# Kernel tuning notes

Hardware: AMD Instinct MI355X
Metric: run time of the kernel (lower is better)

The kernel has to match this reference:

```python
import jax, jax.numpy as jnp
import numpy as np

EPS = 1e-3  # tfa GroupNormalization default epsilon
H = 8       # num heads


def group_norm(x, gamma, beta):
    # x: [..., E]; per-sample group norm over each group of head_dim channels
    lead, E = x.shape[:-1], x.shape[-1]
    D = E // H
    xg = x.reshape(lead + (H, D))
    mu = xg.mean(-1, keepdims=True)
    var = xg.var(-1, keepdims=True)
    xg = (xg - mu) * jax.lax.rsqrt(var + EPS)
    xg = xg * gamma.reshape(H, D) + beta.reshape(H, D)
    return xg.reshape(lead + (E,))


def in_proj(x, W, b, gamma, beta):
    # Dense -> CELU(alpha=1) == ELU -> GroupNorm(groups=H)
    return group_norm(jax.nn.elu(x @ W + b), gamma, beta)


def setup_inputs() -> dict:
    B, M, E, MID = 16, 2048, 1024, 64
    D = E // H
    ks = jax.random.split(jax.random.key(0), 16)
    w = lambda k, shape: jax.random.normal(k, shape, jnp.float32) * 0.02
    inp = {
        "query": jax.random.normal(ks[0], (B, E), jnp.float32),
        "key": jax.random.normal(ks[1], (B * M, E), jnp.float32),
        "mask": jnp.ones((B, M), jnp.float32),
        "value1": jax.random.normal(ks[2], (B, E), jnp.float32),
        "value2": jax.random.normal(ks[3], (B * M, E), jnp.float32),
        # four in-projection layers: Dense(E,E) + GroupNorm gamma/beta
        "Wq": w(ks[4], (E, E)), "bq": jnp.zeros((E,), jnp.float32), "gq": jnp.ones((E,), jnp.float32), "Bq": jnp.zeros((E,), jnp.float32),
        "Wk": w(ks[5], (E, E)), "bk": jnp.zeros((E,), jnp.float32), "gk": jnp.ones((E,), jnp.float32), "Bk": jnp.zeros((E,), jnp.float32),
        "Wv1": w(ks[6], (E, E)), "bv1": jnp.zeros((E,), jnp.float32), "gv1": jnp.ones((E,), jnp.float32), "Bv1": jnp.zeros((E,), jnp.float32),
        "Wv2": w(ks[7], (E, E)), "bv2": jnp.zeros((E,), jnp.float32), "gv2": jnp.ones((E,), jnp.float32), "Bv2": jnp.zeros((E,), jnp.float32),
        # XLASCAtt: basic Dense(head_dim->64)+ReLU; last Dense(64->1); last2 Dense(64->head_dim)
        "Wb": w(ks[8], (D, MID)), "bb": jnp.zeros((MID,), jnp.float32),
        "Wl1": w(ks[9], (MID, 1)), "bl1": jnp.zeros((1,), jnp.float32),
        "Wl2": w(ks[10], (MID, D)), "bl2": jnp.zeros((D,), jnp.float32),
    }
    return inp


def reference(query, key, mask, value1, value2,
              Wq, bq, gq, Bq, Wk, bk, gk, Bk,
              Wv1, bv1, gv1, Bv1, Wv2, bv2, gv2, Bv2,
              Wb, bb, Wl1, bl1, Wl2, bl2):
    B, E = query.shape
    D = E // H
    # in-projections
    q = in_proj(query, Wq, bq, gq, Bq).reshape(B, H, D)            # [B,H,D]
    v1 = in_proj(value1, Wv1, bv1, gv1, Bv1).reshape(B, H, D)      # [B,H,D]
    k = in_proj(key, Wk, bk, gk, Bk).reshape(B, -1, H, D).transpose(0, 2, 1, 3)       # [B,H,M,D]
    v2 = in_proj(value2, Wv2, bv2, gv2, Bv2).reshape(B, -1, H, D).transpose(0, 2, 1, 3)  # [B,H,M,D]

    # low-rank bilinear attention map: elementwise q*k per head
    att_map = q[:, :, None, :] * k                                 # [B,H,M,D]
    basic = jax.nn.relu(att_map @ Wb + bb)                         # [B,H,M,MID]

    # masked mean-pool over memory positions
    m_ext = mask[:, None, :, None]                                 # [B,1,M,1]
    pool = (basic * m_ext).sum(-2) / m_ext.sum(-2)                 # [B,H,MID]

    # spatial attention (softmax over M) and channel gate (sigmoid)
    alpha_sp = (basic @ Wl1 + bl1)[..., 0]                         # [B,H,M]
    alpha_sp = jnp.where(mask[:, None, :] == 0, -1e9, alpha_sp)
    alpha_sp = jax.nn.softmax(alpha_sp, axis=-1)
    alpha_ch = jax.nn.sigmoid(pool @ Wl2 + bl2)                    # [B,H,D]

    v2_agg = jnp.einsum('bhm,bhmd->bhd', alpha_sp, v2)             # [B,H,D]
    attn = v1 * v2_agg * alpha_ch                                  # [B,H,D]
    return attn.reshape(B, H * D)
```

## Files before the change

kernel.cpp:

```cpp
#include <hip/hip_runtime.h>
#include <hip/hip_bf16.h>
#include <math.h>

typedef __attribute__((ext_vector_type(8))) short bf16x8;
typedef __attribute__((ext_vector_type(4))) float f32x4;
typedef __attribute__((ext_vector_type(8))) unsigned short u16x8;

typedef const float* fptr;
typedef const unsigned short* bfp;

__device__ inline float b2f(unsigned short u) {
    union { unsigned int i; float f; } v; v.i = ((unsigned int)u) << 16; return v.f;
}
__device__ inline unsigned short f2b(float x) {
    __hip_bfloat16 h = __float2bfloat16(x);
    return *(unsigned short*)&h;
}
__device__ inline float elu_f(float x) { return x > 0.f ? x : __expf(x) - 1.f; }

__device__ inline void load_lds16(const void* g, void* l) {
    __builtin_amdgcn_global_load_lds(
        (const __attribute__((address_space(1))) unsigned int*)g,
        (__attribute__((address_space(3))) unsigned int*)l, 16, 0, 0);
}

__global__ __launch_bounds__(256) void prep(
    fptr key, fptr value2, unsigned short* AbfK, unsigned short* AbfV2,
    fptr Wk, fptr Wv2, unsigned short* WtK, unsigned short* WtV2,
    fptr Wb, unsigned short* Wbt,
    fptr query, fptr Wq, fptr bq, fptr gq, fptr Bq,
    fptr value1, fptr Wv1, fptr bv1, fptr gv1, fptr Bv1,
    float* qws, float* v1ws)
{
    __shared__ __align__(16) char smem[16640];
    int blk = blockIdx.x, t = threadIdx.x;

    if (blk == 0) {
        unsigned short* tb = (unsigned short*)smem;
        for (int i = 0; i < 32; i++) {
            int idx = i * 256 + t;
            tb[(idx & 63) * 128 + (idx >> 6)] = f2b(Wb[idx]);
        }
        __syncthreads();
        for (int i = 0; i < 4; i++) {
            int o = (i * 256 + t) * 8;
            *(u16x8*)&Wbt[o] = *(const u16x8*)&tb[o];
        }
        return;
    }
    if (blk < 257) {
        float* xs = (float*)smem;
        float (*part)[128] = (float (*)[128])(smem + 4096);
        float (*r4)[2] = (float (*)[2])(smem + 4096 + 1024);
        int idx = blk - 1;
        int hgrp = idx & 7;
        int row  = (idx >> 3) & 15;
        int which = idx >> 7;
        fptr x  = which ? value1 : query;
        fptr W  = which ? Wv1 : Wq;
        fptr bi = which ? bv1 : bq;
        fptr g  = which ? gv1 : gq;
        fptr be = which ? Bv1 : Bq;
        float* outp = which ? v1ws : qws;
        int lane = t & 63, wv = t >> 6;
        for (int i = t; i < 1024; i += 256) xs[i] = x[row * 1024 + i];
        __syncthreads();
        int cl = t & 127, kh = t >> 7;
        int col = hgrp * 128 + cl;
        float acc = 0.f;
        const float* wp = W + (size_t)(kh * 512) * 1024 + col;
        for (int k = 0; k < 512; k++) acc += xs[kh * 512 + k] * wp[(size_t)k * 1024];
        part[kh][cl] = acc;
        __syncthreads();
        float e = 0.f;
        if (t < 128) e = elu_f(part[0][t] + part[1][t] + bi[col]);
        float s = e, ss = e * e;
        for (int m = 32; m > 0; m >>= 1) { s += __shfl_xor(s, m); ss += __shfl_xor(ss, m); }
        if (lane == 0) { r4[wv][0] = s; r4[wv][1] = ss; }
        __syncthreads();
        float S  = r4[0][0] + r4[1][0] + r4[2][0] + r4[3][0];
        float SS = r4[0][1] + r4[1][1] + r4[2][1] + r4[3][1];
        float mean = S * (1.f / 128.f);
        float var  = SS * (1.f / 128.f) - mean * mean;
        float inv  = rsqrtf(var + 1e-3f);
        if (t < 128) outp[row * 1024 + col] = (e - mean) * inv * g[col] + be[col];
        return;
    }
    if (blk < 769) {
        float (*tl)[65] = (float (*)[65])smem;
        int idx = blk - 257;
        fptr W = (idx >> 8) ? Wv2 : Wk;
        unsigned short* Wt = (idx >> 8) ? WtV2 : WtK;
        int k0 = ((idx >> 4) & 15) * 64, n0 = (idx & 15) * 64;
        #pragma unroll
        for (int i = 0; i < 16; i++) {
            int kl = i * 4 + (t >> 6), nl = t & 63;
            tl[kl][nl] = W[(size_t)(k0 + kl) * 1024 + n0 + nl];
        }
        __syncthreads();
        #pragma unroll
        for (int i = 0; i < 16; i++) {
            int nl = i * 4 + (t >> 6), kl = t & 63;
            Wt[(size_t)(n0 + nl) * 1024 + k0 + kl] = f2b(tl[kl][nl]);
        }
        return;
    }
    {
        int idx = blk - 769;
        fptr A = (idx < 16384) ? key : value2;
        unsigned short* B = (idx < 16384) ? AbfK : AbfV2;
        size_t e = ((size_t)(idx & 16383) * 256 + t) * 8;
        const float4* ap = (const float4*)(A + e);
        float4 a0 = ap[0], a1 = ap[1];
        u16x8 p = { f2b(a0.x), f2b(a0.y), f2b(a0.z), f2b(a0.w),
                    f2b(a1.x), f2b(a1.y), f2b(a1.z), f2b(a1.w) };
        *(u16x8*)(B + e) = p;
    }
}

__global__ __launch_bounds__(256, 3) void gemm_fused(
    bfp AK, bfp WtK, fptr bkp, fptr gkp, fptr Bkp,
    bfp AV, bfp WtV, fptr bvp, fptr gvp, fptr Bvp,
    bfp Wbt, const float* qws, fptr maskp, fptr bbp, fptr Wl1, fptr bl1,
    float* logits, float* poolpart, __hip_bfloat16* Z)
{
    __shared__ __align__(16) unsigned short pool[17408];
    unsigned short (*As)[128][32] = (unsigned short (*)[128][32])pool;
    unsigned short (*Bs)[128][32] = (unsigned short (*)[128][32])(pool + 8192);
    unsigned short (*Tt)[136]     = (unsigned short (*)[136])pool;
    __shared__ float sstat[128][2][2];
    __shared__ float masksh[128];
    __shared__ float poolred[4][64];

    int bid = blockIdx.x;
    int xcd = bid & 7;
    int seq = bid >> 3;
    int grp = seq >> 3;
    int h   = seq & 7;
    int which = grp >> 5;
    int rowtile = xcd * 32 + (grp & 31);

    int r0 = rowtile * 128;
    int n0 = h * 128;
    int b  = r0 >> 11;
    int mloc = r0 & 2047;
    int mt = rowtile & 15;
    int t = threadIdx.x, lane = t & 63, w = t >> 6;
    int c = lane & 15, q = lane >> 4;
    int rowbase = (w & 1) * 64, colbase = (w >> 1) * 64;

    bfp A    = which ? AV  : AK;
    bfp Wt   = which ? WtV : WtK;
    fptr bias = which ? bvp : bkp;
    fptr g    = which ? gvp : gkp;
    fptr be   = which ? Bvp : Bkp;

    if (which == 0 && t < 128) masksh[t] = maskp[r0 + t];

    f32x4 acc[4][4];
    const f32x4 fzero = {0.f, 0.f, 0.f, 0.f};
    #pragma unroll
    for (int i = 0; i < 4; i++)
        #pragma unroll
        for (int j = 0; j < 4; j++) acc[i][j] = fzero;

    int srow = lane >> 2;
    int sseg = (lane & 3) * 8;
    const unsigned short* ag = A  + (size_t)(r0 + w * 32 + srow) * 1024 + sseg;
    const unsigned short* bg = Wt + (size_t)(n0 + w * 32 + srow) * 1024 + sseg;

    for (int k0 = 0; k0 < 1024; k0 += 64) {
        load_lds16(ag + k0,                  &As[0][w * 32][0]);
        load_lds16(ag + k0 + 16 * 1024,      &As[0][w * 32 + 16][0]);
        load_lds16(ag + k0 + 32,             &As[1][w * 32][0]);
        load_lds16(ag + k0 + 32 + 16 * 1024, &As[1][w * 32 + 16][0]);
        load_lds16(bg + k0,                  &Bs[0][w * 32][0]);
        load_lds16(bg + k0 + 16 * 1024,      &Bs[0][w * 32 + 16][0]);
        load_lds16(bg + k0 + 32,             &Bs[1][w * 32][0]);
        load_lds16(bg + k0 + 32 + 16 * 1024, &Bs[1][w * 32 + 16][0]);
        __syncthreads();
        #pragma unroll
        for (int p = 0; p < 2; p++) {
            bf16x8 af[4], bfv[4];
            #pragma unroll
            for (int i = 0; i < 4; i++) af[i]  = *(const bf16x8*)&As[p][rowbase + i * 16 + c][q * 8];
            #pragma unroll
            for (int j = 0; j < 4; j++) bfv[j] = *(const bf16x8*)&Bs[p][colbase + j * 16 + c][q * 8];
            #pragma unroll
            for (int i = 0; i < 4; i++)
                #pragma unroll
                for (int j = 0; j < 4; j++)
                    acc[i][j] = __builtin_amdgcn_mfma_f32_16x16x32_bf16(af[i], bfv[j], acc[i][j], 0, 0, 0);
        }
        __syncthreads();
    }

    float bcol[4], gcol[4], Bcol[4];
    #pragma unroll
    for (int j = 0; j < 4; j++) {
        int cg = n0 + colbase + j * 16 + c;
        bcol[j] = bias[cg]; gcol[j] = g[cg]; Bcol[j] = be[cg];
    }
    #pragma unroll
    for (int i = 0; i < 4; i++)
        #pragma unroll
        for (int j = 0; j < 4; j++)
            #pragma unroll
            for (int r = 0; r < 4; r++)
                acc[i][j][r] = elu_f(acc[i][j][r] + bcol[j]);
    #pragma unroll
    for (int i = 0; i < 4; i++) {
        #pragma unroll
        for (int r = 0; r < 4; r++) {
            float s  = acc[i][0][r] + acc[i][1][r] + acc[i][2][r] + acc[i][3][r];
            float ss = acc[i][0][r] * acc[i][0][r] + acc[i][1][r] * acc[i][1][r]
                     + acc[i][2][r] * acc[i][2][r] + acc[i][3][r] * acc[i][3][r];
            for (int m = 1; m < 16; m <<= 1) { s += __shfl_xor(s, m); ss += __shfl_xor(ss, m); }
            if (c == 0) {
                int rl = rowbase + i * 16 + q * 4 + r;
                sstat[rl][w >> 1][0] = s;
                sstat[rl][w >> 1][1] = ss;
            }
        }
    }
    __syncthreads();
    #pragma unroll
    for (int i = 0; i < 4; i++) {
        #pragma unroll
        for (int r = 0; r < 4; r++) {
            int rl = rowbase + i * 16 + q * 4 + r;
            float S  = sstat[rl][0][0] + sstat[rl][1][0];
            float SS = sstat[rl][0][1] + sstat[rl][1][1];
            float mean = S * (1.f / 128.f);
            float var  = SS * (1.f / 128.f) - mean * mean;
            float inv  = rsqrtf(var + 1e-3f);
            #pragma unroll
            for (int j = 0; j < 4; j++) {
                int cl = colbase + j * 16 + c;
                float v = (acc[i][j][r] - mean) * inv * gcol[j] + Bcol[j];
                if (which == 0) Tt[rl][cl] = f2b(v);
                else Z[(size_t)(r0 + rl) * 1024 + n0 + cl] = __float2bfloat16(v);
            }
        }
    }
    if (which != 0) return;
    __syncthreads();

    const float* qrow = qws + b * 1024 + h * 128;
    f32x4 acc2[2][4];
    #pragma unroll
    for (int i = 0; i < 2; i++)
        #pragma unroll
        for (int j = 0; j < 4; j++) acc2[i][j] = fzero;
    #pragma unroll
    for (int s = 0; s < 4; s++) {
        bf16x8 af2[2], bfv[4];
        float qv[8];
        #pragma unroll
        for (int e = 0; e < 8; e++) qv[e] = qrow[s * 32 + q * 8 + e];
        #pragma unroll
        for (int i = 0; i < 2; i++)
            af2[i] = *(const bf16x8*)&Tt[w * 32 + i * 16 + c][s * 32 + q * 8];
        #pragma unroll
        for (int j = 0; j < 4; j++) {
            bf16x8 wv = *(const bf16x8*)&Wbt[(j * 16 + c) * 128 + s * 32 + q * 8];
            bf16x8 bv;
            #pragma unroll
            for (int e = 0; e < 8; e++)
                bv[e] = (short)f2b(b2f((unsigned short)wv[e]) * qv[e]);
            bfv[j] = bv;
        }
        #pragma unroll
        for (int i = 0; i < 2; i++)
            #pragma unroll
            for (int j = 0; j < 4; j++)
                acc2[i][j] = __builtin_amdgcn_mfma_f32_16x16x32_bf16(af2[i], bfv[j], acc2[i][j], 0, 0, 0);
    }

    float bbs[4], wl1s[4];
    #pragma unroll
    for (int j = 0; j < 4; j++) { bbs[j] = bbp[j * 16 + c]; wl1s[j] = Wl1[j * 16 + c]; }
    float bl1v = bl1[0];
    float pp[4] = {0.f, 0.f, 0.f, 0.f};
    #pragma unroll
    for (int i = 0; i < 2; i++) {
        #pragma unroll
        for (int r = 0; r < 4; r++) {
            int ml = w * 32 + i * 16 + q * 4 + r;
            float mv = masksh[ml];
            float lg = 0.f;
            #pragma unroll
            for (int j = 0; j < 4; j++) {
                float basic = fmaxf(acc2[i][j][r] + bbs[j], 0.f);
                lg += basic * wl1s[j];
                pp[j] += basic * mv;
            }
            lg += __shfl_xor(lg, 1); lg += __shfl_xor(lg, 2);
            lg += __shfl_xor(lg, 4); lg += __shfl_xor(lg, 8);
            if (c == 0)
                logits[((size_t)(b * 8 + h)) * 2048 + mloc + ml] = lg + bl1v;
        }
    }
    #pragma unroll
    for (int j = 0; j < 4; j++) {
        pp[j] += __shfl_xor(pp[j], 16);
        pp[j] += __shfl_xor(pp[j], 32);
    }
    if (lane < 16) {
        #pragma unroll
        for (int j = 0; j < 4; j++) poolred[w][j * 16 + c] = pp[j];
    }
    __syncthreads();
    if (t < 64) {
        float p = poolred[0][t] + poolred[1][t] + poolred[2][t] + poolred[3][t];
        poolpart[((size_t)((b * 8 + h) * 16 + mt)) * 64 + t] = p;
    }
}

__global__ __launch_bounds__(512) void finalize_fused(
    const float* logits, const float* poolpart, fptr maskp,
    const __hip_bfloat16* v2buf, const float* v1ws,
    fptr Wl2, fptr bl2, float* out)
{
    __shared__ float alph[2048];
    __shared__ float red[8];
    __shared__ float redm[8];
    __shared__ float pools[64];
    __shared__ float ach[128];
    __shared__ float redl[8][128];
    int h = blockIdx.x, b = blockIdx.y;
    int t = threadIdx.x, lane = t & 63, wv = t >> 6;

    const float* lg = logits + (size_t)(b * 8 + h) * 2048;
    float msum_l = 0.f, mx_l = -1e30f;
    for (int i = t; i < 2048; i += 512) {
        float mv = maskp[b * 2048 + i];
        msum_l += mv;
        float v = (mv == 0.f) ? -1e9f : lg[i];
        alph[i] = v;
        mx_l = fmaxf(mx_l, v);
    }
    for (int mm = 32; mm > 0; mm >>= 1) {
        msum_l += __shfl_xor(msum_l, mm);
        mx_l = fmaxf(mx_l, __shfl_xor(mx_l, mm));
    }
    if (lane == 0) { red[wv] = msum_l; redm[wv] = mx_l; }
    __syncthreads();
    float msum = 0.f, mx = -1e30f;
    #pragma unroll
    for (int i = 0; i < 8; i++) { msum += red[i]; mx = fmaxf(mx, redm[i]); }

    float se = 0.f;
    for (int i = t; i < 2048; i += 512) {
        float e = __expf(alph[i] - mx);
        alph[i] = e;
        se += e;
    }
    for (int mm = 32; mm > 0; mm >>= 1) se += __shfl_xor(se, mm);
    __syncthreads();
    if (lane == 0) red[wv] = se;
    __syncthreads();
    float S = 0.f;
    #pragma unroll
    for (int i = 0; i < 8; i++) S += red[i];
    float invS = 1.f / S;
    for (int i = t; i < 2048; i += 512) alph[i] *= invS;

    if (t < 64) {
        const float* pq = poolpart + ((size_t)(b * 8 + h) * 16) * 64 + t;
        float p = 0.f;
        for (int pt = 0; pt < 16; pt++) p += pq[pt * 64];
        pools[t] = p / msum;
    }
    __syncthreads();
    if (t < 128) {
        float s2 = bl2[t];
        for (int mid = 0; mid < 64; mid++) s2 += pools[mid] * Wl2[mid * 128 + t];
        ach[t] = 1.f / (1.f + __expf(-s2));
    }
    __syncthreads();

    int mo = lane >> 4, d8 = (lane & 15) * 8;
    float acc[8] = {};
    for (int it = 0; it < 64; it++) {
        int m = it * 32 + wv * 4 + mo;
        bf16x8 v8 = *(const bf16x8*)&v2buf[((size_t)(b * 2048 + m)) * 1024 + h * 128 + d8];
        float a = alph[m];
        #pragma unroll
        for (int j = 0; j < 8; j++)
            acc[j] += a * b2f(((unsigned short*)&v8)[j]);
    }
    #pragma unroll
    for (int j = 0; j < 8; j++) {
        acc[j] += __shfl_xor(acc[j], 16);
        acc[j] += __shfl_xor(acc[j], 32);
    }
    if (lane < 16) {
        #pragma unroll
        for (int j = 0; j < 8; j++) redl[wv][d8 + j] = acc[j];
    }
    __syncthreads();
    if (t < 128) {
        float s = 0.f;
        #pragma unroll
        for (int i = 0; i < 8; i++) s += redl[i][t];
        out[b * 1024 + h * 128 + t] = v1ws[b * 1024 + h * 128 + t] * s * ach[t];
    }
}

extern "C" void kernel_launch(void* const* d_in, const int* in_sizes, int n_in,
                              void* d_out, int out_size, void* d_ws, size_t ws_size,
                              hipStream_t stream) {
    fptr query  = (fptr)d_in[0];
    fptr key    = (fptr)d_in[1];
    fptr maskp  = (fptr)d_in[2];
    fptr value1 = (fptr)d_in[3];
    fptr value2 = (fptr)d_in[4];
    fptr Wq = (fptr)d_in[5],  bq = (fptr)d_in[6],  gq = (fptr)d_in[7],  Bq = (fptr)d_in[8];
    fptr Wk = (fptr)d_in[9],  bk = (fptr)d_in[10], gk = (fptr)d_in[11], Bk = (fptr)d_in[12];
    fptr Wv1 = (fptr)d_in[13], bv1 = (fptr)d_in[14], gv1 = (fptr)d_in[15], Bv1 = (fptr)d_in[16];
    fptr Wv2 = (fptr)d_in[17], bv2 = (fptr)d_in[18], gv2 = (fptr)d_in[19], Bv2 = (fptr)d_in[20];
    fptr Wb = (fptr)d_in[21], bb = (fptr)d_in[22];
    fptr Wl1 = (fptr)d_in[23], bl1 = (fptr)d_in[24];
    fptr Wl2 = (fptr)d_in[25], bl2 = (fptr)d_in[26];

    const size_t MB = 1024 * 1024;
    char* w = (char*)d_ws;
    unsigned short* AbfK  = (unsigned short*)w;
    unsigned short* AbfV2 = (unsigned short*)(w + 64 * MB);
    __hip_bfloat16* zV2   = (__hip_bfloat16*)(w + 128 * MB);
    unsigned short* WtK   = (unsigned short*)(w + 192 * MB);
    unsigned short* WtV2  = (unsigned short*)(w + 194 * MB);
    unsigned short* Wbt   = (unsigned short*)(w + 196 * MB);
    float* qws      = (float*)(w + 196 * MB + 65536 + 2 * MB);
    float* v1ws     = qws + 16 * 1024;
    float* logits   = v1ws + 16 * 1024;
    float* poolpart = logits + 16 * 8 * 2048;
    float* out = (float*)d_out;

    hipLaunchKernelGGL(prep, dim3(33537), dim3(256), 0, stream,
                       key, value2, AbfK, AbfV2,
                       Wk, Wv2, WtK, WtV2, Wb, Wbt,
                       query, Wq, bq, gq, Bq, value1, Wv1, bv1, gv1, Bv1,
                       qws, v1ws);
    hipLaunchKernelGGL(gemm_fused, dim3(4096), dim3(256), 0, stream,
                       (bfp)AbfK, (bfp)WtK, bk, gk, Bk,
                       (bfp)AbfV2, (bfp)WtV2, bv2, gv2, Bv2,
                       (bfp)Wbt, qws, maskp, bb, Wl1, bl1, logits, poolpart, zV2);
    hipLaunchKernelGGL(finalize_fused, dim3(8, 16), dim3(512), 0, stream,
                       logits, poolpart, maskp, zV2, v1ws, Wl2, bl2, out);
}
```

Baseline: 578.5 us.

## Vectorize weight transpose stores, coarsen bf16 conversion, stage Z writes via LDS

The weight transpose now writes 8 bf16 values per 16-byte store instead of scalar 2-byte stores. The fp32-to-bf16 conversion of key and value2 is coarsened so each block handles 8 chunks, which cuts the prep grid from 33537 to 4865 blocks. In the GEMM, the value2 branch now writes its normalized output tile to LDS first and then copies it out with coalesced 16-byte stores, replacing strided scalar bf16 stores. The GEMM's launch_bounds occupancy hint is raised from 3 to 4 blocks, which may force register spilling.

```diff
diff --git a/kernel.cpp b/kernel.cpp
--- a/kernel.cpp
+++ b/kernel.cpp
@@ -99,26 +99,33 @@
         }
         __syncthreads();
         #pragma unroll
-        for (int i = 0; i < 16; i++) {
-            int nl = i * 4 + (t >> 6), kl = t & 63;
-            Wt[(size_t)(n0 + nl) * 1024 + k0 + kl] = f2b(tl[kl][nl]);
+        for (int i = 0; i < 2; i++) {
+            int nl = i * 32 + (t >> 3), kl8 = (t & 7) * 8;
+            u16x8 o;
+            #pragma unroll
+            for (int e = 0; e < 8; e++) o[e] = f2b(tl[kl8 + e][nl]);
+            *(u16x8*)&Wt[(size_t)(n0 + nl) * 1024 + k0 + kl8] = o;
         }
         return;
     }
     {
         int idx = blk - 769;
-        fptr A = (idx < 16384) ? key : value2;
-        unsigned short* B = (idx < 16384) ? AbfK : AbfV2;
-        size_t e = ((size_t)(idx & 16383) * 256 + t) * 8;
-        const float4* ap = (const float4*)(A + e);
-        float4 a0 = ap[0], a1 = ap[1];
-        u16x8 p = { f2b(a0.x), f2b(a0.y), f2b(a0.z), f2b(a0.w),
-                    f2b(a1.x), f2b(a1.y), f2b(a1.z), f2b(a1.w) };
-        *(u16x8*)(B + e) = p;
-    }
-}
-
-__global__ __launch_bounds__(256, 3) void gemm_fused(
+        fptr A = (idx < 2048) ? key : value2;
+        unsigned short* Bp = (idx < 2048) ? AbfK : AbfV2;
+        size_t base = (size_t)(idx & 2047) * 16384 + (size_t)t * 8;
+        #pragma unroll
+        for (int i = 0; i < 8; i++) {
+            size_t e = base + (size_t)i * 2048;
+            const float4* ap = (const float4*)(A + e);
+            float4 a0 = ap[0], a1 = ap[1];
+            u16x8 p = { f2b(a0.x), f2b(a0.y), f2b(a0.z), f2b(a0.w),
+                        f2b(a1.x), f2b(a1.y), f2b(a1.z), f2b(a1.w) };
+            *(u16x8*)(Bp + e) = p;
+        }
+    }
+}
+
+__global__ __launch_bounds__(256, 4) void gemm_fused(
     bfp AK, bfp WtK, fptr bkp, fptr gkp, fptr Bkp,
     bfp AV, bfp WtV, fptr bvp, fptr gvp, fptr Bvp,
     bfp Wbt, const float* qws, fptr maskp, fptr bbp, fptr Wl1, fptr bl1,
@@ -238,13 +245,21 @@
             for (int j = 0; j < 4; j++) {
                 int cl = colbase + j * 16 + c;
                 float v = (acc[i][j][r] - mean) * inv * gcol[j] + Bcol[j];
-                if (which == 0) Tt[rl][cl] = f2b(v);
-                else Z[(size_t)(r0 + rl) * 1024 + n0 + cl] = __float2bfloat16(v);
+                Tt[rl][cl] = f2b(v);
             }
         }
     }
-    if (which != 0) return;
-    __syncthreads();
+    __syncthreads();
+    if (which != 0) {
+        unsigned short* Zu = (unsigned short*)Z;
+        #pragma unroll
+        for (int i = 0; i < 8; i++) {
+            int idx2 = i * 256 + t;
+            int row = idx2 >> 4, ch = (idx2 & 15) * 8;
+            *(u16x8*)&Zu[(size_t)(r0 + row) * 1024 + n0 + ch] = *(const u16x8*)&Tt[row][ch];
+        }
+        return;
+    }
 
     const float* qrow = qws + b * 1024 + h * 128;
     f32x4 acc2[2][4];
@@ -438,7 +453,7 @@
     float* poolpart = logits + 16 * 8 * 2048;
     float* out = (float*)d_out;
 
-    hipLaunchKernelGGL(prep, dim3(33537), dim3(256), 0, stream,
+    hipLaunchKernelGGL(prep, dim3(4865), dim3(256), 0, stream,
                        key, value2, AbfK, AbfV2,
                        Wk, Wv2, WtK, WtV2, Wb, Wbt,
                        query, Wq, bq, gq, Bq, value1, Wv1, bv1, gv1, Bv1,
```

Result: faster. 565.7 us (-2.2%).
